# Kernel optimization log

Hardware: AMD Instinct MI355X
Metric: run time of the kernel (lower is better)

## Reference

```python
import jax, jax.numpy as jnp
import numpy as np

NUM_GROUPS = 32
EPS = 1e-6


def group_norm(x, gamma, beta):
    # x: [B, C, H, W]
    b, c, h, w = x.shape
    xg = x.reshape(b, NUM_GROUPS, c // NUM_GROUPS, h, w)
    mean = xg.mean(axis=(2, 3, 4), keepdims=True)
    var = xg.var(axis=(2, 3, 4), keepdims=True)
    xn = ((xg - mean) * jax.lax.rsqrt(var + EPS)).reshape(b, c, h, w)
    return xn * gamma[None, :, None, None] + beta[None, :, None, None]


def setup_inputs() -> dict:
    key = jax.random.key(0)
    ks = jax.random.split(key, 10)
    B, C, H, W = 2, 512, 64, 64
    s = 1.0 / np.sqrt(C)
    return {
        "x": jax.random.normal(ks[0], (B, C, H, W), dtype=jnp.float32),
        "gamma": jnp.ones((C,), jnp.float32),
        "beta": jnp.zeros((C,), jnp.float32),
        "Wq": jax.random.normal(ks[1], (C, C), jnp.float32) * s,
        "bq": jnp.zeros((C,), jnp.float32),
        "Wk": jax.random.normal(ks[2], (C, C), jnp.float32) * s,
        "bk": jnp.zeros((C,), jnp.float32),
        "Wv": jax.random.normal(ks[3], (C, C), jnp.float32) * s,
        "bv": jnp.zeros((C,), jnp.float32),
        "Wo": jax.random.normal(ks[4], (C, C), jnp.float32) * s,
        "bo": jnp.zeros((C,), jnp.float32),
    }


def reference(x, gamma, beta, Wq, bq, Wk, bk, Wv, bv, Wo, bo):
    b, c, h, w = x.shape
    hn = group_norm(x, gamma, beta)               # [B,C,H,W]
    hf = hn.reshape(b, c, h * w)                  # [B,C,N]
    # 1x1 convs == channel matmuls
    q = jnp.einsum('oc,bcn->bon', Wq, hf) + bq[None, :, None]
    k = jnp.einsum('oc,bcn->bon', Wk, hf) + bk[None, :, None]
    v = jnp.einsum('oc,bcn->bon', Wv, hf) + bv[None, :, None]
    scale = float(c) ** -0.5
    scores = jnp.einsum('bci,bcj->bij', q, k) * scale   # [B,N,N]
    attn = jax.nn.softmax(scores, axis=-1)
    out = jnp.einsum('bij,bcj->bci', attn, v)            # [B,C,N]
    out = jnp.einsum('oc,bcn->bon', Wo, out) + bo[None, :, None]
    return x + out.reshape(b, c, h, w)
```

## Files before the change

### kernel.cpp

```cpp
#include <hip/hip_runtime.h>

#define BB 2
#define CC 512
#define NS 4096
#define NGROUP 32
#define TILE 128
#define RSTRIDE 132

typedef __bf16 bf16_8 __attribute__((ext_vector_type(8)));
typedef __bf16 bf16_4 __attribute__((ext_vector_type(4)));
typedef float f32_4 __attribute__((ext_vector_type(4)));

#define SMEM_BYTES 65536
#define SMEM256 131072

__device__ __forceinline__ void gld_lds16(const __bf16* g, __bf16* l) {
  __builtin_amdgcn_global_load_lds(
      (const __attribute__((address_space(1))) unsigned int*)g,
      (__attribute__((address_space(3))) unsigned int*)l, 16, 0, 0);
}

__global__ __launch_bounds__(256) void gn_stats(const float* __restrict__ x,
                                                float* __restrict__ stats) {
  const float4* p = (const float4*)(x + (size_t)blockIdx.x * 65536);
  float s = 0.f, q = 0.f;
  for (int i = threadIdx.x; i < 16384; i += 256) {
    float4 v = p[i];
    s += v.x + v.y + v.z + v.w;
    q += v.x * v.x + v.y * v.y + v.z * v.z + v.w * v.w;
  }
#pragma unroll
  for (int off = 32; off > 0; off >>= 1) {
    s += __shfl_down(s, off, 64);
    q += __shfl_down(q, off, 64);
  }
  __shared__ float ls[4], lq[4];
  int wave = threadIdx.x >> 6, lane = threadIdx.x & 63;
  if (lane == 0) { ls[wave] = s; lq[wave] = q; }
  __syncthreads();
  if (threadIdx.x == 0) {
    float S = ls[0] + ls[1] + ls[2] + ls[3];
    float Q = lq[0] + lq[1] + lq[2] + lq[3];
    float mean = S * (1.f / 65536.f);
    float var = Q * (1.f / 65536.f) - mean * mean;
    stats[blockIdx.x * 2] = mean;
    stats[blockIdx.x * 2 + 1] = rsqrtf(var + 1e-6f);
  }
}

__global__ __launch_bounds__(256) void gn_apply_t(const float* __restrict__ x,
                                                  const float* __restrict__ stats,
                                                  const float* __restrict__ gamma,
                                                  const float* __restrict__ beta,
                                                  __bf16* __restrict__ hnT) {
  __shared__ float tile[32][33];
  int b = blockIdx.z;
  int c0 = blockIdx.y * 32;
  int n0 = blockIdx.x * 32;
  int tx = threadIdx.x;
  int ty = threadIdx.y;
  const float* xb = x + (size_t)b * CC * NS;
#pragma unroll
  for (int i = 0; i < 4; i++) {
    int c = c0 + ty + i * 8;
    float mean = stats[(b * NGROUP + (c >> 4)) * 2 + 0];
    float rstd = stats[(b * NGROUP + (c >> 4)) * 2 + 1];
    float v = xb[(size_t)c * NS + n0 + tx];
    tile[ty + i * 8][tx] = (v - mean) * rstd * gamma[c] + beta[c];
  }
  __syncthreads();
  __bf16* out = hnT + (size_t)b * NS * CC;
#pragma unroll
  for (int i = 0; i < 4; i++) {
    int n = n0 + ty + i * 8;
    out[(size_t)n * CC + c0 + tx] = (__bf16)tile[tx][ty + i * 8];
  }
}

__global__ __launch_bounds__(256) void cvt_w(const float* __restrict__ w0, const float* __restrict__ w1,
                                             const float* __restrict__ w2, const float* __restrict__ w3,
                                             __bf16* __restrict__ o0, __bf16* __restrict__ o1,
                                             __bf16* __restrict__ o2, __bf16* __restrict__ o3) {
  int tsel = blockIdx.x >> 8;
  int i = (blockIdx.x & 255) * 256 + threadIdx.x;
  const float* src = tsel == 0 ? w0 : tsel == 1 ? w1 : tsel == 2 ? w2 : w3;
  __bf16* dst = tsel == 0 ? o0 : tsel == 1 ? o1 : tsel == 2 ? o2 : o3;
  float4 v = ((const float4*)src)[i];
  bf16_4 r;
  r[0] = (__bf16)v.x; r[1] = (__bf16)v.y; r[2] = (__bf16)v.z; r[3] = (__bf16)v.w;
  ((bf16_4*)dst)[i] = r;
}

__device__ __forceinline__ void gemm_core8(const __bf16* __restrict__ A, const __bf16* __restrict__ B,
                                           int K, int lda, int ldb,
                                           __bf16* lds, f32_4 (&acc)[4][2]) {
  const int t = threadIdx.x;
  const int lane = t & 63;
  const int wave = t >> 6;
  const int lrow = lane & 15, quad = lane >> 4;
  const int wrow = (wave >> 2) * 64, wcol = (wave & 3) * 32;
  const int co = (quad ^ ((lrow >> 1) & 3)) * 8;
  const int r0 = t >> 2;
  const int kp = ((t & 3) ^ ((t >> 3) & 3)) * 8;
  const __bf16* pA = A + (size_t)r0 * lda + kp;
  const __bf16* pB = B + (size_t)r0 * ldb + kp;
  {
    __bf16* lA = lds;
    __bf16* lB = lds + 8192;
    gld_lds16(pA,      &lA[t * 8]);
    gld_lds16(pA + 32, &lA[4096 + t * 8]);
    gld_lds16(pB,      &lB[t * 8]);
    gld_lds16(pB + 32, &lB[4096 + t * 8]);
  }
  int buf = 0;
  for (int k0 = 0; k0 < K; k0 += 64, buf ^= 1) {
    __syncthreads();
    if (k0 + 64 < K) {
      __bf16* lA = lds + (buf ^ 1) * 16384;
      __bf16* lB = lA + 8192;
      gld_lds16(pA + k0 + 64, &lA[t * 8]);
      gld_lds16(pA + k0 + 96, &lA[4096 + t * 8]);
      gld_lds16(pB + k0 + 64, &lB[t * 8]);
      gld_lds16(pB + k0 + 96, &lB[4096 + t * 8]);
    }
    const __bf16* bA = lds + buf * 16384;
    const __bf16* bB = bA + 8192;
#pragma unroll
    for (int ks = 0; ks < 2; ks++) {
      const __bf16* la = bA + ks * 4096;
      const __bf16* lb = bB + ks * 4096;
      bf16_8 af[4], bfr[2];
#pragma unroll
      for (int i = 0; i < 4; i++)
        af[i] = *(const bf16_8*)&la[(wrow + i * 16 + lrow) * 32 + co];
#pragma unroll
      for (int j = 0; j < 2; j++)
        bfr[j] = *(const bf16_8*)&lb[(wcol + j * 16 + lrow) * 32 + co];
#pragma unroll
      for (int i = 0; i < 4; i++)
#pragma unroll
        for (int j = 0; j < 2; j++)
          acc[i][j] = __builtin_amdgcn_mfma_f32_16x16x32_bf16(af[i], bfr[j], acc[i][j], 0, 0, 0);
    }
  }
}

__device__ __forceinline__ void stage_acc8(float* ls, const f32_4 (&acc)[4][2], int pass) {
  const int t = threadIdx.x;
  const int lane = t & 63, wave = t >> 6;
  const int lrow = lane & 15, quad = lane >> 4;
  const int wrow = (wave >> 2) * 64, wcol = (wave & 3) * 32;
  if ((wrow >> 6) == pass) {
#pragma unroll
    for (int i = 0; i < 4; i++)
#pragma unroll
      for (int r = 0; r < 4; r++)
#pragma unroll
        for (int jj = 0; jj < 2; jj++)
          ls[(i * 16 + quad * 4 + r) * RSTRIDE + wcol + jj * 16 + lrow] = acc[i][jj][r];
  }
}

__device__ __forceinline__ void drain_bf16_8(const float* ls, __bf16* gdst, int ldg) {
  const int t = threadIdx.x;
#pragma unroll
  for (int k2 = 0; k2 < 4; k2++) {
    int idx = k2 * 512 + t;
    int row = idx >> 5, col = (idx & 31) * 4;
    f32_4 v = *(const f32_4*)&ls[row * RSTRIDE + col];
    bf16_4 o;
    o[0] = (__bf16)v[0]; o[1] = (__bf16)v[1]; o[2] = (__bf16)v[2]; o[3] = (__bf16)v[3];
    *(bf16_4*)&gdst[(size_t)row * ldg + col] = o;
  }
}

__device__ __forceinline__ void gemm_core256(const __bf16* __restrict__ A,
                                             const __bf16* __restrict__ B,
                                             int K, int lda, int ldb,
                                             __bf16* lds, f32_4 (&acc)[8][4]) {
  const int t = threadIdx.x;
  const int lane = t & 63;
  const int wave = t >> 6;
  const int lrow = lane & 15, quad = lane >> 4;
  const int wm = wave >> 2, wn = wave & 3;
  const int r0 = t >> 2;
  const int kp = ((t & 3) ^ ((t >> 3) & 3)) * 8;
  const __bf16* gA0 = A + (size_t)r0 * lda + kp;
  const __bf16* gA1 = A + (size_t)(r0 + 128) * lda + kp;
  const __bf16* gB0 = B + (size_t)r0 * ldb + kp;
  const __bf16* gB1 = B + (size_t)(r0 + 128) * ldb + kp;
  const int co = (quad ^ ((lrow >> 1) & 3)) * 8;
  const int aoff = (wm * 128 + lrow) * 32 + co;
  const int boff = 16384 + (wn * 64 + lrow) * 32 + co;
  const int KT = K >> 6;

#define STG(bufv, isB, srcp, hh, ktv)                                         \
  {                                                                           \
    __bf16* d_ = lds + (bufv) * 32768 + (isB) * 16384 + (hh) * 4096 + t * 8;  \
    const __bf16* s_ = (srcp) + (ktv) * 64;                                   \
    gld_lds16(s_, d_);                                                        \
    gld_lds16(s_ + 32, d_ + 8192);                                            \
  }
#define LOAD_AF(IH)                                                           \
  _Pragma("unroll") for (int i = 0; i < 4; i++)                               \
      _Pragma("unroll") for (int ks = 0; ks < 2; ks++)                        \
          af[i][ks] = *(const bf16_8*)&bb[aoff + ((IH) * 4 + i) * 512 + ks * 8192];
#define LOAD_BV(J0)                                                           \
  _Pragma("unroll") for (int j = 0; j < 2; j++)                               \
      _Pragma("unroll") for (int ks = 0; ks < 2; ks++)                        \
          bv[(J0) + j][ks] = *(const bf16_8*)&bb[boff + ((J0) + j) * 512 + ks * 8192];
#define MFMA16(I0, J0)                                                        \
  _Pragma("unroll") for (int ks = 0; ks < 2; ks++)                            \
      _Pragma("unroll") for (int i = 0; i < 4; i++)                           \
          _Pragma("unroll") for (int j = 0; j < 2; j++)                       \
              acc[(I0) + i][(J0) + j] = __builtin_amdgcn_mfma_f32_16x16x32_bf16( \
                  af[i][ks], bv[(J0) + j][ks], acc[(I0) + i][(J0) + j], 0, 0, 0);
#define PHASE_BEGIN()                                                         \
  __builtin_amdgcn_s_barrier();                                               \
  asm volatile("s_waitcnt lgkmcnt(0)" ::: "memory");                          \
  __builtin_amdgcn_sched_barrier(0);                                          \
  __builtin_amdgcn_s_setprio(1);
#define PHASE_END()                                                           \
  __builtin_amdgcn_s_setprio(0);                                              \
  __builtin_amdgcn_s_barrier();

  STG(0, 0, gA0, 0, 0)
  STG(0, 0, gA1, 1, 0)
  STG(0, 1, gB0, 0, 0)
  STG(0, 1, gB1, 1, 0)
  STG(1, 1, gB0, 0, 1)
  STG(1, 1, gB1, 1, 1)
  asm volatile("s_waitcnt vmcnt(4)" ::: "memory");
  __builtin_amdgcn_s_barrier();

  for (int it = 0; it < (KT >> 1); ++it) {
#pragma unroll
    for (int h = 0; h < 2; ++h) {
      const int kt = 2 * it + h;
      const __bf16* bb = lds + h * 32768;
      bf16_8 af[4][2], bv[4][2];
      LOAD_AF(0)
      LOAD_BV(0)
      if (kt + 1 < KT) STG(h ^ 1, 0, gA0, 0, kt + 1)
      PHASE_BEGIN()
      MFMA16(0, 0)
      PHASE_END()
      LOAD_BV(2)
      if (kt + 1 < KT) STG(h ^ 1, 0, gA1, 1, kt + 1)
      PHASE_BEGIN()
      MFMA16(0, 2)
      PHASE_END()
      LOAD_AF(1)
      if (kt + 2 < KT) STG(h, 1, gB0, 0, kt + 2)
      PHASE_BEGIN()
      MFMA16(4, 0)
      PHASE_END()
      if (kt + 2 < KT) STG(h, 1, gB1, 1, kt + 2)
      PHASE_BEGIN()
      MFMA16(4, 2)
      __builtin_amdgcn_s_setprio(0);
      if (kt + 2 < KT) {
        asm volatile("s_waitcnt vmcnt(4)" ::: "memory");
      } else {
        asm volatile("s_waitcnt vmcnt(0)" ::: "memory");
      }
      __builtin_amdgcn_s_barrier();
    }
  }
#undef STG
#undef LOAD_AF
#undef LOAD_BV
#undef MFMA16
#undef PHASE_BEGIN
#undef PHASE_END
}

__device__ __forceinline__ void gemm_coreF(const __bf16* __restrict__ A,
                                           const __bf16* __restrict__ B,
                                           int K, int lda, int ldb,
                                           __bf16* lds, f32_4 (&acc)[8][4]) {
  const int t = threadIdx.x;
  const int lane = t & 63;
  const int wave = t >> 6;
  const int lrow = lane & 15, quad = lane >> 4;
  const int wm = wave >> 2, wn = wave & 3;
  const int r0 = t >> 2;
  const int kp = ((t & 3) ^ ((t >> 3) & 3)) * 8;
  const __bf16* gA0 = A + (size_t)r0 * lda + kp;
  const __bf16* gA1 = A + (size_t)(r0 + 128) * lda + kp;
  const __bf16* gB0 = B + (size_t)r0 * ldb + kp;
  const __bf16* gB1 = B + (size_t)(r0 + 128) * ldb + kp;
  const int co = (quad ^ ((lrow >> 1) & 3)) * 8;
  const int aoff = (wm * 128 + lrow) * 32 + co;
  const int boff = 16384 + (wn * 64 + lrow) * 32 + co;
  const int KT = K >> 6;

  {
    __bf16* d = lds + t * 8;
    gld_lds16(gA0,      d);
    gld_lds16(gA1,      d + 4096);
    gld_lds16(gA0 + 32, d + 8192);
    gld_lds16(gA1 + 32, d + 12288);
    gld_lds16(gB0,      d + 16384);
    gld_lds16(gB1,      d + 20480);
    gld_lds16(gB0 + 32, d + 24576);
    gld_lds16(gB1 + 32, d + 28672);
  }
  int buf = 0;
  for (int kt = 0; kt < KT; ++kt, buf ^= 1) {
    __syncthreads();
    if (kt + 1 < KT) {
      __bf16* d = lds + (buf ^ 1) * 32768 + t * 8;
      const int go = (kt + 1) * 64;
      gld_lds16(gA0 + go,      d);
      gld_lds16(gA1 + go,      d + 4096);
      gld_lds16(gA0 + go + 32, d + 8192);
      gld_lds16(gA1 + go + 32, d + 12288);
      gld_lds16(gB0 + go,      d + 16384);
      gld_lds16(gB1 + go,      d + 20480);
      gld_lds16(gB0 + go + 32, d + 24576);
      gld_lds16(gB1 + go + 32, d + 28672);
    }
    const __bf16* bb = lds + buf * 32768;
#pragma unroll
    for (int ks = 0; ks < 2; ks++) {
      bf16_8 af[8], bv[4];
#pragma unroll
      for (int f = 0; f < 8; f++)
        af[f] = *(const bf16_8*)&bb[aoff + f * 512 + ks * 8192];
#pragma unroll
      for (int j = 0; j < 4; j++)
        bv[j] = *(const bf16_8*)&bb[boff + j * 512 + ks * 8192];
#pragma unroll
      for (int f = 0; f < 8; f++)
#pragma unroll
        for (int j = 0; j < 4; j++)
          acc[f][j] = __builtin_amdgcn_mfma_f32_16x16x32_bf16(af[f], bv[j], acc[f][j], 0, 0, 0);
    }
  }
}

__global__ __launch_bounds__(512, 2) void e_gemm256(const __bf16* __restrict__ qT,
                                                    const __bf16* __restrict__ kT,
                                                    __bf16* __restrict__ E,
                                                    float* __restrict__ l,
                                                    float scale) {
  extern __shared__ __bf16 ldsdyn[];
  const int bid = blockIdx.x;
  const int lin = (bid & 7) * 64 + (bid >> 3);
  const int b = lin >> 8;
  const int rm = lin & 255;
  const int R = rm >> 5, s = rm & 31;
  const int mt = (R >> 2) * 8 + (s >> 2);
  const int nt = (R & 3) * 4 + (s & 3);
  const int m0 = mt * 256, n0 = nt * 256;
  const long long sBNC = (long long)NS * CC;
  const long long sBNN = (long long)NS * NS;
  const __bf16* Ap = qT + (size_t)b * sBNC + (size_t)m0 * CC;
  const __bf16* Bp = kT + (size_t)b * sBNC + (size_t)n0 * CC;

  f32_4 acc[8][4];
#pragma unroll
  for (int i = 0; i < 8; i++)
#pragma unroll
    for (int j = 0; j < 4; j++) acc[i][j] = {0.f, 0.f, 0.f, 0.f};

  gemm_coreF(Ap, Bp, CC, CC, CC, ldsdyn, acc);

  const int t = threadIdx.x;
  const int lane = t & 63, wave = t >> 6;
  const int lrow = lane & 15, quad = lane >> 4;
  const int wm = wave >> 2, wn = wave & 3;
  __bf16* Ep = E + (size_t)b * sBNN;
  float* lp = l + (size_t)b * NS;
#pragma unroll
  for (int i = 0; i < 8; i++) {
#pragma unroll
    for (int r = 0; r < 4; r++) {
      int gm = m0 + wm * 128 + i * 16 + quad * 4 + r;
      float rp = 0.f;
#pragma unroll
      for (int j = 0; j < 4; j++) {
        int gn = n0 + wn * 64 + j * 16 + lrow;
        float ev = __expf(acc[i][j][r] * scale);
        rp += ev;
        Ep[(size_t)gm * NS + gn] = (__bf16)ev;
      }
      rp += __shfl_down(rp, 8, 16);
      rp += __shfl_down(rp, 4, 16);
      rp += __shfl_down(rp, 2, 16);
      rp += __shfl_down(rp, 1, 16);
      if (lrow == 0) atomicAdd(&lp[gm], rp);
    }
  }
}

__global__ __launch_bounds__(512, 2) void ao256(const __bf16* __restrict__ E,
                                                const __bf16* __restrict__ vv,
                                                __bf16* __restrict__ p0,
                                                __bf16* __restrict__ p1,
                                                __bf16* __restrict__ p2,
                                                __bf16* __restrict__ p3) {
  extern __shared__ __bf16 ldsdyn[];
  const int bid = blockIdx.x;
  const int lin = (bid & 7) * 32 + (bid >> 3);
  const int split = lin >> 6;
  const int rem = lin & 63;
  const int b = rem >> 5;
  const int mt = (rem & 31) >> 1;
  const int nt = rem & 1;
  const int m0 = mt * 256, n0 = nt * 256;
  const long long sBNN = (long long)NS * NS;
  const long long sBCN = (long long)CC * NS;
  const long long sBNC = (long long)NS * CC;
  const __bf16* Ap = E + (size_t)b * sBNN + (size_t)m0 * NS + (size_t)split * 1024;
  const __bf16* Bp = vv + (size_t)b * sBCN + (size_t)n0 * NS + (size_t)split * 1024;
  __bf16* Cp = (split == 0 ? p0 : split == 1 ? p1 : split == 2 ? p2 : p3) + (size_t)b * sBNC;

  f32_4 acc[8][4];
#pragma unroll
  for (int i = 0; i < 8; i++)
#pragma unroll
    for (int j = 0; j < 4; j++) acc[i][j] = {0.f, 0.f, 0.f, 0.f};

  gemm_core256(Ap, Bp, 1024, NS, NS, ldsdyn, acc);

  const int t = threadIdx.x;
  const int lane = t & 63, wave = t >> 6;
  const int lrow = lane & 15, quad = lane >> 4;
  const int wm = wave >> 2, wn = wave & 3;
#pragma unroll
  for (int i = 0; i < 8; i++) {
#pragma unroll
    for (int r = 0; r < 4; r++) {
      int gm = m0 + wm * 128 + i * 16 + quad * 4 + r;
#pragma unroll
      for (int j = 0; j < 4; j++) {
        int gn = n0 + wn * 64 + j * 16 + lrow;
        Cp[(size_t)gm * CC + gn] = (__bf16)acc[i][j][r];
      }
    }
  }
}

__global__ __launch_bounds__(512, 4) void qkv_gemm(const __bf16* __restrict__ hnT,
                                                   const __bf16* __restrict__ Wq,
                                                   const __bf16* __restrict__ Wk,
                                                   const __bf16* __restrict__ Wv,
                                                   const float* __restrict__ bq,
                                                   const float* __restrict__ bk,
                                                   const float* __restrict__ bv,
                                                   __bf16* __restrict__ qT,
                                                   __bf16* __restrict__ kT,
                                                   __bf16* __restrict__ vv) {
  __shared__ char smem[SMEM_BYTES];
  __bf16* lds = (__bf16*)smem;
  float* lsr = (float*)smem;
  const int b = blockIdx.z;
  const int id = blockIdx.x;
  const int sel = id >> 7;
  const int r = id & 127;
  const long long sBNC = (long long)NS * CC;
  const long long sBCN = (long long)CC * NS;

  int m0, n0, N;
  const __bf16 *Ap, *Bp;
  __bf16* Cp;
  const float* bias;
  if (sel < 2) {
    m0 = (r >> 2) * TILE;
    n0 = (r & 3) * TILE;
    Ap = hnT + (size_t)b * sBNC + (size_t)m0 * CC;
    Bp = (sel == 0 ? Wq : Wk) + (size_t)n0 * CC;
    Cp = (sel == 0 ? qT : kT) + (size_t)b * sBNC;
    bias = (sel == 0 ? bq : bk);
    N = CC;
  } else {
    m0 = (r & 3) * TILE;
    n0 = (r >> 2) * TILE;
    Ap = Wv + (size_t)m0 * CC;
    Bp = hnT + (size_t)b * sBNC + (size_t)n0 * CC;
    Cp = vv + (size_t)b * sBCN;
    bias = bv;
    N = NS;
  }

  f32_4 acc[4][2];
#pragma unroll
  for (int i = 0; i < 4; i++)
#pragma unroll
    for (int j = 0; j < 2; j++) acc[i][j] = {0.f, 0.f, 0.f, 0.f};

  gemm_core8(Ap, Bp, CC, CC, CC, lds, acc);

  const int t = threadIdx.x;
  const int lane = t & 63;
  const int lrow = lane & 15, quad = lane >> 4;
  const int wave = t >> 6;
  const int wrow = (wave >> 2) * 64, wcol = (wave & 3) * 32;
#pragma unroll
  for (int i = 0; i < 4; i++)
#pragma unroll
    for (int r2 = 0; r2 < 4; r2++) {
      float rowb = (sel == 2) ? bias[m0 + wrow + i * 16 + quad * 4 + r2] : 0.f;
#pragma unroll
      for (int j = 0; j < 2; j++) {
        float cb = (sel < 2) ? bias[n0 + wcol + j * 16 + lrow] : rowb;
        acc[i][j][r2] += cb;
      }
    }

#pragma unroll
  for (int p = 0; p < 2; p++) {
    __syncthreads();
    stage_acc8(lsr, acc, p);
    __syncthreads();
    drain_bf16_8(lsr, Cp + (size_t)(m0 + p * 64) * N + n0, N);
  }
}

__global__ __launch_bounds__(256) void reduce_ao4(const __bf16* __restrict__ p0,
                                                  const __bf16* __restrict__ p1,
                                                  const __bf16* __restrict__ p2,
                                                  const __bf16* __restrict__ p3,
                                                  const float* __restrict__ l,
                                                  __bf16* __restrict__ o) {
  int i = blockIdx.x * 256 + threadIdx.x;
  int row = i >> 6;
  float inv = 1.f / l[row];
  bf16_8 a = ((const bf16_8*)p0)[i];
  bf16_8 c = ((const bf16_8*)p1)[i];
  bf16_8 d = ((const bf16_8*)p2)[i];
  bf16_8 e = ((const bf16_8*)p3)[i];
  bf16_8 r;
#pragma unroll
  for (int k = 0; k < 8; k++)
    r[k] = (__bf16)(((float)a[k] + (float)c[k] + (float)d[k] + (float)e[k]) * inv);
  ((bf16_8*)o)[i] = r;
}

__global__ __launch_bounds__(512, 4) void wo_full(const __bf16* __restrict__ Wo,
                                                  const __bf16* __restrict__ aoT,
                                                  __bf16* __restrict__ pw0) {
  __shared__ char smem[SMEM_BYTES];
  __bf16* lds = (__bf16*)smem;
  float* lsr = (float*)smem;
  const int b = blockIdx.z;
  const int m0 = blockIdx.y * TILE;
  const int n0 = blockIdx.x * TILE;
  const long long sBNC = (long long)NS * CC;
  const long long sBCN = (long long)CC * NS;
  const __bf16* Ap = Wo + (size_t)m0 * CC;
  const __bf16* Bp = aoT + (size_t)b * sBNC + (size_t)n0 * CC;
  __bf16* Cp = pw0 + (size_t)b * sBCN;

  f32_4 acc[4][2];
#pragma unroll
  for (int i = 0; i < 4; i++)
#pragma unroll
    for (int j = 0; j < 2; j++) acc[i][j] = {0.f, 0.f, 0.f, 0.f};

  gemm_core8(Ap, Bp, CC, CC, CC, lds, acc);

#pragma unroll
  for (int p = 0; p < 2; p++) {
    __syncthreads();
    stage_acc8(lsr, acc, p);
    __syncthreads();
    drain_bf16_8(lsr, Cp + (size_t)(m0 + p * 64) * NS + n0, NS);
  }
}

__global__ __launch_bounds__(256) void final_out(const __bf16* __restrict__ pw0,
                                                 const float* __restrict__ bo,
                                                 const float* __restrict__ x,
                                                 float* __restrict__ out) {
  int i = blockIdx.x * 256 + threadIdx.x;
  int o = (i >> 10) & (CC - 1);
  float bias = bo[o];
  bf16_4 a = ((const bf16_4*)pw0)[i];
  float4 xr = ((const float4*)x)[i];
  float4 r;
  r.x = (float)a[0] + bias + xr.x;
  r.y = (float)a[1] + bias + xr.y;
  r.z = (float)a[2] + bias + xr.z;
  r.w = (float)a[3] + bias + xr.w;
  ((float4*)out)[i] = r;
}

extern "C" void kernel_launch(void* const* d_in, const int* in_sizes, int n_in,
                              void* d_out, int out_size, void* d_ws, size_t ws_size,
                              hipStream_t stream) {
  const float* x = (const float*)d_in[0];
  const float* gamma = (const float*)d_in[1];
  const float* beta = (const float*)d_in[2];
  const float* Wq = (const float*)d_in[3];
  const float* bq = (const float*)d_in[4];
  const float* Wk = (const float*)d_in[5];
  const float* bk = (const float*)d_in[6];
  const float* Wv = (const float*)d_in[7];
  const float* bv = (const float*)d_in[8];
  const float* Wo = (const float*)d_in[9];
  const float* bo = (const float*)d_in[10];
  float* out = (float*)d_out;

  char* ws = (char*)d_ws;
  __bf16* hnT = (__bf16*)(ws + 0);
  __bf16* qT  = (__bf16*)(ws + 8388608);
  __bf16* kT  = (__bf16*)(ws + 16777216);
  __bf16* vv  = (__bf16*)(ws + 25165824);
  __bf16* aoT = (__bf16*)(ws + 33554432);
  __bf16* Eb  = (__bf16*)(ws + 41943040);
  __bf16* pw0 = (__bf16*)(ws + 41943040);
  __bf16* Wqb = (__bf16*)(ws + 109051904);
  __bf16* Wkb = (__bf16*)(ws + 109576192);
  __bf16* Wvb = (__bf16*)(ws + 110100480);
  __bf16* Wob = (__bf16*)(ws + 110624768);
  float* stats = (float*)(ws + 111149056);
  float* lsum = (float*)(ws + 109051904);
  __bf16* p0 = hnT;
  __bf16* p1 = qT;
  __bf16* p2 = kT;
  __bf16* p3 = aoT;

  const float scale = 0.044194173824159216f;

  static int smem_attr_set = 0;
  if (!smem_attr_set) {
    hipFuncSetAttribute(reinterpret_cast<const void*>(e_gemm256),
                        hipFuncAttributeMaxDynamicSharedMemorySize, SMEM256);
    hipFuncSetAttribute(reinterpret_cast<const void*>(ao256),
                        hipFuncAttributeMaxDynamicSharedMemorySize, SMEM256);
    smem_attr_set = 1;
  }

  cvt_w<<<1024, 256, 0, stream>>>(Wq, Wk, Wv, Wo, Wqb, Wkb, Wvb, Wob);
  gn_stats<<<BB * NGROUP, 256, 0, stream>>>(x, stats);
  gn_apply_t<<<dim3(NS / 32, CC / 32, BB), dim3(32, 8), 0, stream>>>(x, stats, gamma, beta, hnT);

  qkv_gemm<<<dim3(384, 1, BB), 512, 0, stream>>>(hnT, Wqb, Wkb, Wvb, bq, bk, bv, qT, kT, vv);

  hipMemsetAsync(lsum, 0, BB * NS * sizeof(float), stream);
  e_gemm256<<<512, 512, SMEM256, stream>>>(qT, kT, Eb, lsum, scale);

  ao256<<<256, 512, SMEM256, stream>>>(Eb, vv, p0, p1, p2, p3);
  reduce_ao4<<<2048, 256, 0, stream>>>(p0, p1, p2, p3, lsum, aoT);

  wo_full<<<dim3(NS / TILE, CC / TILE, BB), 512, 0, stream>>>(Wob, aoT, pw0);
  final_out<<<4096, 256, 0, stream>>>(pw0, bo, x, out);
}
```

Measured before the change: 242.4 us.

## Fuse output projection epilogue with bias and residual; split GN stats across blocks

The Wo GEMM epilogue now adds the bias and the residual x and writes the fp32 output directly. This removes the bf16 intermediate buffer and the separate final_out kernel, along with one round trip of reads and writes. Group-norm statistics are now computed by four blocks per group, which atomically accumulate sum and sum-of-squares into a buffer zeroed by cvt_w, so more CUs work on that small reduction. The mean and rstd are then finalised in gn_apply_t, with the added risks that the atomic ordering makes the sums nondeterministic and the zeroing depends on cvt_w running first.

```diff
diff --git a/kernel.cpp b/kernel.cpp
--- a/kernel.cpp
+++ b/kernel.cpp
@@ -20,11 +20,13 @@
       (__attribute__((address_space(3))) unsigned int*)l, 16, 0, 0);
 }
 
-__global__ __launch_bounds__(256) void gn_stats(const float* __restrict__ x,
-                                                float* __restrict__ stats) {
-  const float4* p = (const float4*)(x + (size_t)blockIdx.x * 65536);
+__global__ __launch_bounds__(256) void gn_stats2(const float* __restrict__ x,
+                                                 float* __restrict__ st) {
+  const int g = blockIdx.x >> 2;
+  const int ch = blockIdx.x & 3;
+  const float4* p = (const float4*)(x + (size_t)g * 65536 + (size_t)ch * 16384);
   float s = 0.f, q = 0.f;
-  for (int i = threadIdx.x; i < 16384; i += 256) {
+  for (int i = threadIdx.x; i < 4096; i += 256) {
     float4 v = p[i];
     s += v.x + v.y + v.z + v.w;
     q += v.x * v.x + v.y * v.y + v.z * v.z + v.w * v.w;
@@ -41,15 +43,13 @@
   if (threadIdx.x == 0) {
     float S = ls[0] + ls[1] + ls[2] + ls[3];
     float Q = lq[0] + lq[1] + lq[2] + lq[3];
-    float mean = S * (1.f / 65536.f);
-    float var = Q * (1.f / 65536.f) - mean * mean;
-    stats[blockIdx.x * 2] = mean;
-    stats[blockIdx.x * 2 + 1] = rsqrtf(var + 1e-6f);
+    atomicAdd(&st[g * 2], S);
+    atomicAdd(&st[g * 2 + 1], Q);
   }
 }
 
 __global__ __launch_bounds__(256) void gn_apply_t(const float* __restrict__ x,
-                                                  const float* __restrict__ stats,
+                                                  const float* __restrict__ st,
                                                   const float* __restrict__ gamma,
                                                   const float* __restrict__ beta,
                                                   __bf16* __restrict__ hnT) {
@@ -63,8 +63,11 @@
 #pragma unroll
   for (int i = 0; i < 4; i++) {
     int c = c0 + ty + i * 8;
-    float mean = stats[(b * NGROUP + (c >> 4)) * 2 + 0];
-    float rstd = stats[(b * NGROUP + (c >> 4)) * 2 + 1];
+    float S = st[(b * NGROUP + (c >> 4)) * 2 + 0];
+    float Q = st[(b * NGROUP + (c >> 4)) * 2 + 1];
+    float mean = S * (1.f / 65536.f);
+    float var = Q * (1.f / 65536.f) - mean * mean;
+    float rstd = rsqrtf(var + 1e-6f);
     float v = xb[(size_t)c * NS + n0 + tx];
     tile[ty + i * 8][tx] = (v - mean) * rstd * gamma[c] + beta[c];
   }
@@ -80,7 +83,9 @@
 __global__ __launch_bounds__(256) void cvt_w(const float* __restrict__ w0, const float* __restrict__ w1,
                                              const float* __restrict__ w2, const float* __restrict__ w3,
                                              __bf16* __restrict__ o0, __bf16* __restrict__ o1,
-                                             __bf16* __restrict__ o2, __bf16* __restrict__ o3) {
+                                             __bf16* __restrict__ o2, __bf16* __restrict__ o3,
+                                             float* __restrict__ stz) {
+  if (blockIdx.x == 0 && threadIdx.x < 128) stz[threadIdx.x] = 0.f;
   int tsel = blockIdx.x >> 8;
   int i = (blockIdx.x & 255) * 256 + threadIdx.x;
   const float* src = tsel == 0 ? w0 : tsel == 1 ? w1 : tsel == 2 ? w2 : w3;
@@ -539,9 +544,11 @@
   ((bf16_8*)o)[i] = r;
 }
 
-__global__ __launch_bounds__(512, 4) void wo_full(const __bf16* __restrict__ Wo,
-                                                  const __bf16* __restrict__ aoT,
-                                                  __bf16* __restrict__ pw0) {
+__global__ __launch_bounds__(512, 4) void wo_fused(const __bf16* __restrict__ Wo,
+                                                   const __bf16* __restrict__ aoT,
+                                                   const float* __restrict__ bo,
+                                                   const float* __restrict__ x,
+                                                   float* __restrict__ out) {
   __shared__ char smem[SMEM_BYTES];
   __bf16* lds = (__bf16*)smem;
   float* lsr = (float*)smem;
@@ -552,7 +559,8 @@
   const long long sBCN = (long long)CC * NS;
   const __bf16* Ap = Wo + (size_t)m0 * CC;
   const __bf16* Bp = aoT + (size_t)b * sBNC + (size_t)n0 * CC;
-  __bf16* Cp = pw0 + (size_t)b * sBCN;
+  const float* xb = x + (size_t)b * sBCN;
+  float* ob = out + (size_t)b * sBCN;
 
   f32_4 acc[4][2];
 #pragma unroll
@@ -562,30 +570,28 @@
 
   gemm_core8(Ap, Bp, CC, CC, CC, lds, acc);
 
+  const int t = threadIdx.x;
 #pragma unroll
   for (int p = 0; p < 2; p++) {
     __syncthreads();
     stage_acc8(lsr, acc, p);
     __syncthreads();
-    drain_bf16_8(lsr, Cp + (size_t)(m0 + p * 64) * NS + n0, NS);
-  }
-}
-
-__global__ __launch_bounds__(256) void final_out(const __bf16* __restrict__ pw0,
-                                                 const float* __restrict__ bo,
-                                                 const float* __restrict__ x,
-                                                 float* __restrict__ out) {
-  int i = blockIdx.x * 256 + threadIdx.x;
-  int o = (i >> 10) & (CC - 1);
-  float bias = bo[o];
-  bf16_4 a = ((const bf16_4*)pw0)[i];
-  float4 xr = ((const float4*)x)[i];
-  float4 r;
-  r.x = (float)a[0] + bias + xr.x;
-  r.y = (float)a[1] + bias + xr.y;
-  r.z = (float)a[2] + bias + xr.z;
-  r.w = (float)a[3] + bias + xr.w;
-  ((float4*)out)[i] = r;
+#pragma unroll
+    for (int k2 = 0; k2 < 4; k2++) {
+      int idx = k2 * 512 + t;
+      int row = idx >> 5, col = (idx & 31) * 4;
+      int o = m0 + p * 64 + row;
+      f32_4 v = *(const f32_4*)&lsr[row * RSTRIDE + col];
+      float bias = bo[o];
+      float4 xr = *(const float4*)&xb[(size_t)o * NS + n0 + col];
+      float4 rr;
+      rr.x = v[0] + bias + xr.x;
+      rr.y = v[1] + bias + xr.y;
+      rr.z = v[2] + bias + xr.z;
+      rr.w = v[3] + bias + xr.w;
+      *(float4*)&ob[(size_t)o * NS + n0 + col] = rr;
+    }
+  }
 }
 
 extern "C" void kernel_launch(void* const* d_in, const int* in_sizes, int n_in,
@@ -611,7 +617,6 @@
   __bf16* vv  = (__bf16*)(ws + 25165824);
   __bf16* aoT = (__bf16*)(ws + 33554432);
   __bf16* Eb  = (__bf16*)(ws + 41943040);
-  __bf16* pw0 = (__bf16*)(ws + 41943040);
   __bf16* Wqb = (__bf16*)(ws + 109051904);
   __bf16* Wkb = (__bf16*)(ws + 109576192);
   __bf16* Wvb = (__bf16*)(ws + 110100480);
@@ -634,8 +639,8 @@
     smem_attr_set = 1;
   }
 
-  cvt_w<<<1024, 256, 0, stream>>>(Wq, Wk, Wv, Wo, Wqb, Wkb, Wvb, Wob);
-  gn_stats<<<BB * NGROUP, 256, 0, stream>>>(x, stats);
+  cvt_w<<<1024, 256, 0, stream>>>(Wq, Wk, Wv, Wo, Wqb, Wkb, Wvb, Wob, stats);
+  gn_stats2<<<4 * BB * NGROUP, 256, 0, stream>>>(x, stats);
   gn_apply_t<<<dim3(NS / 32, CC / 32, BB), dim3(32, 8), 0, stream>>>(x, stats, gamma, beta, hnT);
 
   qkv_gemm<<<dim3(384, 1, BB), 512, 0, stream>>>(hnT, Wqb, Wkb, Wvb, bq, bk, bv, qT, kT, vv);
@@ -646,6 +651,5 @@
   ao256<<<256, 512, SMEM256, stream>>>(Eb, vv, p0, p1, p2, p3);
   reduce_ao4<<<2048, 256, 0, stream>>>(p0, p1, p2, p3, lsum, aoT);
 
-  wo_full<<<dim3(NS / TILE, CC / TILE, BB), 512, 0, stream>>>(Wob, aoT, pw0);
-  final_out<<<4096, 256, 0, stream>>>(pw0, bo, x, out);
-}
+  wo_fused<<<dim3(NS / TILE, CC / TILE, BB), 512, 0, stream>>>(Wob, aoT, bo, x, out);
+}
```

Result: faster. 227.7 us (-6.0%).
